# Kernel optimization log

Hardware: AMD Instinct MI355X
Metric: run time of the kernel (lower is better)

Reference implementation:

```python
import jax, jax.numpy as jnp
import numpy as np


def setup_inputs() -> dict:
    key = jax.random.key(0)
    k1, k2 = jax.random.split(key)
    B, S, D, N = 2, 2048, 1024, 16
    a = jax.random.uniform(k1, (B, S, D, N), dtype=jnp.float32)  # decay coeffs in [0,1)
    b = jax.random.normal(k2, (B, S, D, N), dtype=jnp.float32)
    return {"a": a, "b": b}


def reference(a, b):
    """h[t] = a[t] * h[t-1] + b[t], h[-1] = 0, computed via parallel associative scan.

    Associative op: (a1, b1) * (a2, b2) = (a1 * a2, a2 * b1 + b2).
    With h0 = 0, the running b-component equals h[t] exactly.
    """
    def combine(x, y):
        a1, b1 = x
        a2, b2 = y
        return a1 * a2, a2 * b1 + b2

    _, h = jax.lax.associative_scan(combine, (a, b), axis=1)
    return h  # (batch, seq_len, d_model, d_state)
```

## Files before the change

### kernel.cpp

```cpp
#include <hip/hip_runtime.h>


constexpr int S_LEN        = 2048;
constexpr int DN           = 1024 * 16;
constexpr long BATCH_STRIDE = (long)S_LEN * DN;
constexpr int NCHAIN       = 2 * DN;
constexpr int U            = 16;

__global__ __launch_bounds__(64) void scan_chain_kernel(
    const float* __restrict__ a,
    const float* __restrict__ b,
    float* __restrict__ out)
{
    const int m  = blockIdx.x * 64 + threadIdx.x;
    const int bi = m >> 14;
    const int dn = m & (DN - 1);
    const size_t base = (size_t)bi * BATCH_STRIDE + dn;

    const float* __restrict__ ap = a + base;
    const float* __restrict__ bp = b + base;
    float* __restrict__ op = out + base;

    float abuf[U], bbuf[U];
    #pragma unroll
    for (int u = 0; u < U; ++u) {
        abuf[u] = ap[(size_t)u * DN];
        bbuf[u] = bp[(size_t)u * DN];
    }

    float h = 0.0f;
    for (int s0 = 0; s0 < S_LEN; s0 += U) {
        float anxt[U], bnxt[U];
        const int nxt = s0 + U;
        if (nxt < S_LEN) {
            const float* __restrict__ ap2 = ap + (size_t)nxt * DN;
            const float* __restrict__ bp2 = bp + (size_t)nxt * DN;
            #pragma unroll
            for (int u = 0; u < U; ++u) {
                anxt[u] = ap2[(size_t)u * DN];
                bnxt[u] = bp2[(size_t)u * DN];
            }
        }

        float* __restrict__ op2 = op + (size_t)s0 * DN;
        #pragma unroll
        for (int u = 0; u < U; ++u) {
            h = fmaf(abuf[u], h, bbuf[u]);
            op2[(size_t)u * DN] = h;
        }

        #pragma unroll
        for (int u = 0; u < U; ++u) {
            abuf[u] = anxt[u];
            bbuf[u] = bnxt[u];
        }
    }
}

extern "C" void kernel_launch(void* const* d_in, const int* in_sizes, int n_in,
                              void* d_out, int out_size, void* d_ws, size_t ws_size,
                              hipStream_t stream) {
    const float* a = (const float*)d_in[0];
    const float* b = (const float*)d_in[1];
    float* out = (float*)d_out;

    dim3 grid(NCHAIN / 64);
    dim3 block(64);
    scan_chain_kernel<<<grid, block, 0, stream>>>(a, b, out);
}
```

Before: 583.6 us.

## Double-buffer chunk loads two ahead and use nontemporal output stores

Replaces the single prefetch-then-copy register buffer with two ping-pong register buffers, so loads for chunk k+2 are issued while chunk k+1 is computed and the per-iteration copy is removed. Output stores become nontemporal so they do not pollute the cache. More loads are in flight per thread, which may help hide memory latency in this bandwidth-bound scan, but register use roughly doubles and that may lower occupancy.

```diff
diff --git a/kernel.cpp b/kernel.cpp
--- a/kernel.cpp
+++ b/kernel.cpp
@@ -1,11 +1,32 @@
 #include <hip/hip_runtime.h>
 
 
-constexpr int S_LEN        = 2048;
-constexpr int DN           = 1024 * 16;
+constexpr int S_LEN         = 2048;
+constexpr int DN            = 1024 * 16;
 constexpr long BATCH_STRIDE = (long)S_LEN * DN;
-constexpr int NCHAIN       = 2 * DN;
-constexpr int U            = 16;
+constexpr int NCHAIN        = 2 * DN;
+constexpr int U             = 16;
+constexpr int NIT           = S_LEN / U;
+
+__device__ __forceinline__ void load_batch(const float* __restrict__ ap,
+                                           const float* __restrict__ bp,
+                                           size_t off, float* av, float* bv) {
+    #pragma unroll
+    for (int u = 0; u < U; ++u) {
+        av[u] = ap[off + (size_t)u * DN];
+        bv[u] = bp[off + (size_t)u * DN];
+    }
+}
+
+__device__ __forceinline__ float compute_batch(float h, const float* av, const float* bv,
+                                               float* __restrict__ op, size_t off) {
+    #pragma unroll
+    for (int u = 0; u < U; ++u) {
+        h = fmaf(av[u], h, bv[u]);
+        __builtin_nontemporal_store(h, &op[off + (size_t)u * DN]);
+    }
+    return h;
+}
 
 __global__ __launch_bounds__(64) void scan_chain_kernel(
     const float* __restrict__ a,
@@ -21,40 +42,23 @@
     const float* __restrict__ bp = b + base;
     float* __restrict__ op = out + base;
 
-    float abuf[U], bbuf[U];
-    #pragma unroll
-    for (int u = 0; u < U; ++u) {
-        abuf[u] = ap[(size_t)u * DN];
-        bbuf[u] = bp[(size_t)u * DN];
-    }
+    const size_t step = (size_t)U * DN;
+
+    float a0[U], b0[U], a1[U], b1[U];
+    load_batch(ap, bp, 0,    a0, b0);
+    load_batch(ap, bp, step, a1, b1);
 
     float h = 0.0f;
-    for (int s0 = 0; s0 < S_LEN; s0 += U) {
-        float anxt[U], bnxt[U];
-        const int nxt = s0 + U;
-        if (nxt < S_LEN) {
-            const float* __restrict__ ap2 = ap + (size_t)nxt * DN;
-            const float* __restrict__ bp2 = bp + (size_t)nxt * DN;
-            #pragma unroll
-            for (int u = 0; u < U; ++u) {
-                anxt[u] = ap2[(size_t)u * DN];
-                bnxt[u] = bp2[(size_t)u * DN];
-            }
-        }
-
-        float* __restrict__ op2 = op + (size_t)s0 * DN;
-        #pragma unroll
-        for (int u = 0; u < U; ++u) {
-            h = fmaf(abuf[u], h, bbuf[u]);
-            op2[(size_t)u * DN] = h;
-        }
-
-        #pragma unroll
-        for (int u = 0; u < U; ++u) {
-            abuf[u] = anxt[u];
-            bbuf[u] = bnxt[u];
-        }
+    size_t offC = 0;
+    for (int k = 0; k < NIT - 2; k += 2) {
+        h = compute_batch(h, a0, b0, op, offC);
+        load_batch(ap, bp, offC + 2 * step, a0, b0);
+        h = compute_batch(h, a1, b1, op, offC + step);
+        load_batch(ap, bp, offC + 3 * step, a1, b1);
+        offC += 2 * step;
     }
+    h = compute_batch(h, a0, b0, op, offC);
+    h = compute_batch(h, a1, b1, op, offC + step);
 }
 
 extern "C" void kernel_launch(void* const* d_in, const int* in_sizes, int n_in,
```

Result: slower. 597.9 us (+2.5%).
